# Kernel tuning notes

Measured on AMD Instinct MI355X. Metric: run time of the kernel, lower is better.

## Reference

```python
import jax, jax.numpy as jnp
import numpy as np

N_ATOMS = 500_000
N_BONDS = 1_000_000
NODE, EDGE, OUT = 128, 64, 128
N_PER_DEG = 125_000
DEGREES = (1, 2, 3, 4)
BN_EPS = 1e-5


def setup_inputs() -> dict:
    key = jax.random.key(0)
    ks = jax.random.split(key, 12)
    inp = {
        "atom_repr": jax.random.normal(ks[0], (N_ATOMS, NODE), dtype=jnp.float32),
        "bond_repr": jax.random.normal(ks[1], (N_BONDS, EDGE), dtype=jnp.float32),
    }
    for i, d in enumerate(DEGREES):
        inp[f"atom_idx_d{d}"] = jax.random.randint(jax.random.fold_in(ks[2], i), (N_PER_DEG, d), 0, N_ATOMS, dtype=jnp.int32)
        inp[f"bond_idx_d{d}"] = jax.random.randint(jax.random.fold_in(ks[3], i), (N_PER_DEG, d), 0, N_BONDS, dtype=jnp.int32)
        inp[f"W_d{d}"] = jax.random.normal(jax.random.fold_in(ks[4], i), (OUT, NODE + EDGE), dtype=jnp.float32) / np.sqrt(NODE + EDGE)
    inp["W_self"] = jax.random.normal(ks[5], (OUT, NODE), dtype=jnp.float32) / np.sqrt(NODE)
    inp["bias"] = jnp.zeros((1, OUT), dtype=jnp.float32)
    return inp


def reference(atom_repr, bond_repr,
              atom_idx_d1, atom_idx_d2, atom_idx_d3, atom_idx_d4,
              bond_idx_d1, bond_idx_d2, bond_idx_d3, bond_idx_d4,
              W_d1, W_d2, W_d3, W_d4, W_self, bias):
    atom_idxs = (atom_idx_d1, atom_idx_d2, atom_idx_d3, atom_idx_d4)
    bond_idxs = (bond_idx_d1, bond_idx_d2, bond_idx_d3, bond_idx_d4)
    Ws = (W_d1, W_d2, W_d3, W_d4)
    acts = []
    for aidx, bidx, W in zip(atom_idxs, bond_idxs, Ws):
        a = atom_repr[aidx].sum(axis=1)      # [n_d, NODE] gather+sum over neighbors
        b = bond_repr[bidx].sum(axis=1)      # [n_d, EDGE]
        stacked = jnp.concatenate([a, b], axis=1)  # [n_d, NODE+EDGE]
        acts.append(stacked @ W.T)           # [n_d, OUT]
    neighbor_repr = jnp.concatenate(acts, axis=0)  # [N_ATOMS, OUT]
    self_repr = atom_repr @ W_self.T               # [N_ATOMS, OUT]
    x = self_repr + neighbor_repr + bias
    # BatchNorm1d(affine=False), training mode: biased batch stats
    mean = jnp.mean(x, axis=0)
    var = jnp.var(x, axis=0)
    x = (x - mean) * jax.lax.rsqrt(var + BN_EPS)
    return jax.nn.relu(x)
```

## Files before the change

### kernel.cpp

```cpp
#include <hip/hip_runtime.h>

#define NODE 128
#define EDGE 64
#define OUTC 128
#define KTOT 320
#define NPD 125000
#define N_ATOMS_C 500000
#define BROWS 32
#define NB 8
#define NCHUNK 489
#define LDST 328
#define BN_EPS 1e-5f

typedef short bf16x8 __attribute__((ext_vector_type(8)));
typedef float floatx4 __attribute__((ext_vector_type(4)));

__device__ __forceinline__ unsigned short f2bf(float f) {
    unsigned u = __float_as_uint(f);
    u += 0x7fffu + ((u >> 16) & 1u);
    return (unsigned short)(u >> 16);
}
__device__ __forceinline__ unsigned pack2(float a, float b) {
    return (unsigned)f2bf(a) | ((unsigned)f2bf(b) << 16);
}
__device__ __forceinline__ void add4(float4& a, const float4 b) {
    a.x += b.x; a.y += b.y; a.z += b.z; a.w += b.w;
}

__global__ __launch_bounds__(256) void pack_weights_kernel(
    const float* __restrict__ w1, const float* __restrict__ w2,
    const float* __restrict__ w3, const float* __restrict__ w4,
    const float* __restrict__ W_self, float* __restrict__ stats,
    unsigned short* __restrict__ Wcat)
{
    if (blockIdx.x == 0 && threadIdx.x < 256) stats[threadIdx.x] = 0.f;
    const int idx = blockIdx.x * 256 + threadIdx.x;
    if (idx >= 4 * OUTC * KTOT) return;
    const int d   = idx / (OUTC * KTOT);
    const int rem = idx % (OUTC * KTOT);
    const int n = rem / KTOT, k = rem % KTOT;
    const float* wd = (d == 0) ? w1 : (d == 1) ? w2 : (d == 2) ? w3 : w4;
    const float v = (k < NODE) ? W_self[n * NODE + k]
                               : wd[n * (NODE + EDGE) + (k - NODE)];
    Wcat[idx] = f2bf(v);
}

__global__ __launch_bounds__(256, 2) void compute_x_kernel(
    const float* __restrict__ atom_repr, const float* __restrict__ bond_repr,
    const int* __restrict__ a1, const int* __restrict__ b1,
    const int* __restrict__ a2, const int* __restrict__ b2,
    const int* __restrict__ a3, const int* __restrict__ b3,
    const int* __restrict__ a4, const int* __restrict__ b4,
    const unsigned short* __restrict__ Wcat, const float* __restrict__ bias,
    float* __restrict__ out, float* __restrict__ stats)
{
    const int seg   = blockIdx.x & 3;
    const int chunk = blockIdx.x >> 2;
    const int deg = seg + 1;
    const int* aidx = (seg == 0) ? a1 : (seg == 1) ? a2 : (seg == 2) ? a3 : a4;
    const int* bidx = (seg == 0) ? b1 : (seg == 1) ? b2 : (seg == 2) ? b3 : b4;

    __shared__ unsigned short s_feat[2][BROWS][LDST];
    __shared__ float s_sum[OUTC], s_sq[OUTC];

    const int tid = threadIdx.x;
    if (tid < OUTC) { s_sum[tid] = 0.f; s_sq[tid] = 0.f; }

    const int w    = tid >> 6;
    const int lane = tid & 63;
    const int quad = lane >> 4;
    const int lrow = lane & 15;

    bf16x8 breg[2][10];
    {
        const unsigned short* Wc = Wcat + (size_t)seg * OUTC * KTOT;
        #pragma unroll
        for (int nt = 0; nt < 2; ++nt) {
            const int n = w * 32 + nt * 16 + lrow;
            #pragma unroll
            for (int ks = 0; ks < 10; ++ks) {
                const int k0 = quad * 8 + ks * 32;
                breg[nt][ks] = *reinterpret_cast<const bf16x8*>(Wc + n * KTOT + k0);
            }
        }
    }
    float bias_v[2];
    bias_v[0] = bias[w * 32 + lrow];
    bias_v[1] = bias[w * 32 + 16 + lrow];

    float lsum[2] = {0.f, 0.f}, lsq[2] = {0.f, 0.f};

    const int gr = tid >> 3;
    const int gt = tid & 7;
    const float4* ar = (const float4*)atom_repr;
    const float4* br = (const float4*)bond_repr;

    float4 st_s[4];
    float4 st_a[16];
    float4 st_b[8];

    auto issue = [&](int b) {
        const int r0 = chunk * (BROWS * NB) + b * BROWS + gr;
        const int rc = (r0 < NPD) ? r0 : 0;
        const size_t gi = (size_t)(seg * NPD) + rc;
        int ai[4], bi[4];
        #pragma unroll
        for (int j = 0; j < 4; ++j)
            if (j < deg) { ai[j] = aidx[rc * deg + j]; bi[j] = bidx[rc * deg + j]; }
        #pragma unroll
        for (int h = 0; h < 2; ++h) {
            const int c = h * 16 + gt * 2;
            st_s[h * 2 + 0] = ar[gi * 32 + c];
            st_s[h * 2 + 1] = ar[gi * 32 + c + 1];
            #pragma unroll
            for (int j = 0; j < 4; ++j)
                if (j < deg) {
                    st_a[j * 4 + h * 2 + 0] = ar[(size_t)ai[j] * 32 + c];
                    st_a[j * 4 + h * 2 + 1] = ar[(size_t)ai[j] * 32 + c + 1];
                }
        }
        const int cb = gt * 2;
        #pragma unroll
        for (int j = 0; j < 4; ++j)
            if (j < deg) {
                st_b[j * 2 + 0] = br[(size_t)bi[j] * 16 + cb];
                st_b[j * 2 + 1] = br[(size_t)bi[j] * 16 + cb + 1];
            }
    };

    issue(0);

    for (int b = 0; b < NB; ++b) {
        const int base = chunk * (BROWS * NB) + b * BROWS;
        if (base >= NPD) break;

        {
            unsigned short (*sf)[LDST] = s_feat[b & 1];
            #pragma unroll
            for (int h = 0; h < 2; ++h) {
                const int k0 = h * 64 + gt * 8;
                uint4 p;
                p.x = pack2(st_s[h * 2].x, st_s[h * 2].y);
                p.y = pack2(st_s[h * 2].z, st_s[h * 2].w);
                p.z = pack2(st_s[h * 2 + 1].x, st_s[h * 2 + 1].y);
                p.w = pack2(st_s[h * 2 + 1].z, st_s[h * 2 + 1].w);
                *reinterpret_cast<uint4*>(&sf[gr][k0]) = p;
                float4 u0 = st_a[h * 2], u1 = st_a[h * 2 + 1];
                #pragma unroll
                for (int j = 1; j < 4; ++j)
                    if (j < deg) { add4(u0, st_a[j * 4 + h * 2]); add4(u1, st_a[j * 4 + h * 2 + 1]); }
                p.x = pack2(u0.x, u0.y); p.y = pack2(u0.z, u0.w);
                p.z = pack2(u1.x, u1.y); p.w = pack2(u1.z, u1.w);
                *reinterpret_cast<uint4*>(&sf[gr][NODE + k0]) = p;
            }
            {
                const int k0 = gt * 8;
                float4 u0 = st_b[0], u1 = st_b[1];
                #pragma unroll
                for (int j = 1; j < 4; ++j)
                    if (j < deg) { add4(u0, st_b[j * 2]); add4(u1, st_b[j * 2 + 1]); }
                uint4 p;
                p.x = pack2(u0.x, u0.y); p.y = pack2(u0.z, u0.w);
                p.z = pack2(u1.x, u1.y); p.w = pack2(u1.z, u1.w);
                *reinterpret_cast<uint4*>(&sf[gr][2 * NODE + k0]) = p;
            }
        }

        if (b + 1 < NB) issue(b + 1);

        asm volatile("s_waitcnt lgkmcnt(0)" ::: "memory");
        __builtin_amdgcn_s_barrier();

        unsigned short (*sfr)[LDST] = s_feat[b & 1];
        floatx4 acc[2][2];
        #pragma unroll
        for (int mt = 0; mt < 2; ++mt)
            #pragma unroll
            for (int nt = 0; nt < 2; ++nt) {
                acc[mt][nt][0] = bias_v[nt]; acc[mt][nt][1] = bias_v[nt];
                acc[mt][nt][2] = bias_v[nt]; acc[mt][nt][3] = bias_v[nt];
            }
        #pragma unroll
        for (int ks = 0; ks < 10; ++ks) {
            bf16x8 af0 = *reinterpret_cast<const bf16x8*>(&sfr[lrow][quad * 8 + ks * 32]);
            bf16x8 af1 = *reinterpret_cast<const bf16x8*>(&sfr[16 + lrow][quad * 8 + ks * 32]);
            acc[0][0] = __builtin_amdgcn_mfma_f32_16x16x32_bf16(af0, breg[0][ks], acc[0][0], 0, 0, 0);
            acc[0][1] = __builtin_amdgcn_mfma_f32_16x16x32_bf16(af0, breg[1][ks], acc[0][1], 0, 0, 0);
            acc[1][0] = __builtin_amdgcn_mfma_f32_16x16x32_bf16(af1, breg[0][ks], acc[1][0], 0, 0, 0);
            acc[1][1] = __builtin_amdgcn_mfma_f32_16x16x32_bf16(af1, breg[1][ks], acc[1][1], 0, 0, 0);
        }

        #pragma unroll
        for (int mt = 0; mt < 2; ++mt) {
            #pragma unroll
            for (int nt = 0; nt < 2; ++nt) {
                const int n = w * 32 + nt * 16 + lrow;
                #pragma unroll
                for (int r = 0; r < 4; ++r) {
                    const int m = mt * 16 + quad * 4 + r;
                    const int row = base + m;
                    if (row < NPD) {
                        const float v = acc[mt][nt][r];
                        out[(size_t)(seg * NPD + row) * OUTC + n] = v;
                        lsum[nt] += v; lsq[nt] += v * v;
                    }
                }
            }
        }
    }

    atomicAdd(&s_sum[w * 32 + lrow], lsum[0]);
    atomicAdd(&s_sq [w * 32 + lrow], lsq[0]);
    atomicAdd(&s_sum[w * 32 + 16 + lrow], lsum[1]);
    atomicAdd(&s_sq [w * 32 + 16 + lrow], lsq[1]);
    __syncthreads();
    if (tid < OUTC) {
        atomicAdd(&stats[tid], s_sum[tid]);
        atomicAdd(&stats[OUTC + tid], s_sq[tid]);
    }
}

__global__ void finalize_stats_kernel(float* stats) {
    const int o = threadIdx.x;
    const float inv_n = 1.0f / (float)N_ATOMS_C;
    const float mean = stats[o] * inv_n;
    const float var  = stats[OUTC + o] * inv_n - mean * mean;
    stats[o] = mean;
    stats[OUTC + o] = rsqrtf(var + BN_EPS);
}

#define BN_TOT (N_ATOMS_C * (OUTC / 4))
#define BN_BLOCKS 2048

__global__ __launch_bounds__(256) void bn_relu_kernel(float* __restrict__ x,
                                                      const float* __restrict__ stats) {
    const int gid = blockIdx.x * 256 + threadIdx.x;
    const int c4 = gid & 31;
    const float4 m = ((const float4*)stats)[c4];
    const float4 s = ((const float4*)stats)[32 + c4];
    const int stride = BN_BLOCKS * 256;
    for (size_t e = (size_t)gid; e < (size_t)BN_TOT; e += stride) {
        float4 v = ((float4*)x)[e];
        v.x = fmaxf((v.x - m.x) * s.x, 0.f);
        v.y = fmaxf((v.y - m.y) * s.y, 0.f);
        v.z = fmaxf((v.z - m.z) * s.z, 0.f);
        v.w = fmaxf((v.w - m.w) * s.w, 0.f);
        ((float4*)x)[e] = v;
    }
}

extern "C" void kernel_launch(void* const* d_in, const int* in_sizes, int n_in,
                              void* d_out, int out_size, void* d_ws, size_t ws_size,
                              hipStream_t stream) {
    const float* atom_repr = (const float*)d_in[0];
    const float* bond_repr = (const float*)d_in[1];
    const int*   a1 = (const int*)d_in[2];
    const int*   b1 = (const int*)d_in[3];
    const float* w1 = (const float*)d_in[4];
    const int*   a2 = (const int*)d_in[5];
    const int*   b2 = (const int*)d_in[6];
    const float* w2 = (const float*)d_in[7];
    const int*   a3 = (const int*)d_in[8];
    const int*   b3 = (const int*)d_in[9];
    const float* w3 = (const float*)d_in[10];
    const int*   a4 = (const int*)d_in[11];
    const int*   b4 = (const int*)d_in[12];
    const float* w4 = (const float*)d_in[13];
    const float* W_self = (const float*)d_in[14];
    const float* bias   = (const float*)d_in[15];

    float* out   = (float*)d_out;
    float* stats = (float*)d_ws;
    unsigned short* Wcat = (unsigned short*)((char*)d_ws + 1024);

    pack_weights_kernel<<<(4 * OUTC * KTOT + 255) / 256, 256, 0, stream>>>(
        w1, w2, w3, w4, W_self, stats, Wcat);

    compute_x_kernel<<<NCHUNK * 4, 256, 0, stream>>>(
        atom_repr, bond_repr, a1, b1, a2, b2, a3, b3, a4, b4,
        Wcat, bias, out, stats);

    finalize_stats_kernel<<<1, 128, 0, stream>>>(stats);

    bn_relu_kernel<<<BN_BLOCKS, 256, 0, stream>>>(out, stats);
}
```

Measured before the change: 834.7 us.

## Pair degree segments per block for load balance and prefetch indices two stages ahead

Each block now handles 128 rows from two degree segments, pairing degree 1 with 4 and degree 2 with 3, so every block does a similar amount of gather work. Indices are loaded two stages ahead and features one stage ahead, which splits the dependent index-then-gather latency chain. The compile-time degrees allow full specialization. The cost is reloading the weight registers in the middle of the block and more live registers from the extra index buffers, which could reduce occupancy.

Result: slower. 861.7 us (+3.2%).

```diff
diff --git a/kernel.cpp b/kernel.cpp
--- a/kernel.cpp
+++ b/kernel.cpp
@@ -7,8 +7,9 @@
 #define NPD 125000
 #define N_ATOMS_C 500000
 #define BROWS 32
-#define NB 8
-#define NCHUNK 489
+#define NBATCH 8
+#define ROWS_PER_PHASE 128
+#define NCHUNK 977
 #define LDST 328
 #define BN_EPS 1e-5f
 
@@ -45,6 +46,199 @@
     Wcat[idx] = f2bf(v);
 }
 
+template<int SP, int SQ>
+__device__ __forceinline__ void run_pair(
+    const float4* __restrict__ ar, const float4* __restrict__ br,
+    const int* __restrict__ aP, const int* __restrict__ bP,
+    const int* __restrict__ aQ, const int* __restrict__ bQ,
+    const unsigned short* __restrict__ Wcat, const float* __restrict__ bias,
+    float* __restrict__ out, float* __restrict__ stats,
+    unsigned short (*s_feat)[BROWS][LDST], float* s_sum, float* s_sq,
+    const int chunk, const int tid)
+{
+    constexpr int DP = SP + 1, DQ = SQ + 1;
+    const int w    = tid >> 6;
+    const int lane = tid & 63;
+    const int quad = lane >> 4;
+    const int lrow = lane & 15;
+    const int gr   = tid >> 3;
+    const int gt   = tid & 7;
+
+    bf16x8 breg[2][10];
+    {
+        const unsigned short* Wc = Wcat + SP * OUTC * KTOT;
+        #pragma unroll
+        for (int nt = 0; nt < 2; ++nt) {
+            const int n = w * 32 + nt * 16 + lrow;
+            #pragma unroll
+            for (int ks = 0; ks < 10; ++ks)
+                breg[nt][ks] = *reinterpret_cast<const bf16x8*>(Wc + n * KTOT + quad * 8 + ks * 32);
+        }
+    }
+    float bias_v[2];
+    bias_v[0] = bias[w * 32 + lrow];
+    bias_v[1] = bias[w * 32 + 16 + lrow];
+    float lsum[2] = {0.f, 0.f}, lsq[2] = {0.f, 0.f};
+
+    float4 st_s[4];
+    float4 st_a[16];
+    float4 st_b[8];
+    int ia[2][4], ib[2][4];
+
+    auto issue_idx = [&](int t) {
+        const int dg = (t < 4) ? DP : DQ;
+        const int* ax = (t < 4) ? aP : aQ;
+        const int* bx = (t < 4) ? bP : bQ;
+        const int r0 = chunk * ROWS_PER_PHASE + (t & 3) * BROWS + gr;
+        const int rc = (r0 < NPD) ? r0 : (NPD - 1);
+        int* ia_ = ia[t & 1]; int* ib_ = ib[t & 1];
+        #pragma unroll
+        for (int j = 0; j < 4; ++j)
+            if (j < dg) { ia_[j] = ax[rc * dg + j]; ib_[j] = bx[rc * dg + j]; }
+    };
+
+    auto issue_feat = [&](int t) {
+        const int dg = (t < 4) ? DP : DQ;
+        const int sg = (t < 4) ? SP : SQ;
+        const int r0 = chunk * ROWS_PER_PHASE + (t & 3) * BROWS + gr;
+        const int rc = (r0 < NPD) ? r0 : (NPD - 1);
+        const size_t gi = (size_t)(sg * NPD) + rc;
+        const int* ia_ = ia[t & 1]; const int* ib_ = ib[t & 1];
+        #pragma unroll
+        for (int h = 0; h < 2; ++h) {
+            const int c = h * 16 + gt * 2;
+            st_s[h * 2 + 0] = ar[gi * 32 + c];
+            st_s[h * 2 + 1] = ar[gi * 32 + c + 1];
+            #pragma unroll
+            for (int j = 0; j < 4; ++j)
+                if (j < dg) {
+                    st_a[j * 4 + h * 2 + 0] = ar[(size_t)ia_[j] * 32 + c];
+                    st_a[j * 4 + h * 2 + 1] = ar[(size_t)ia_[j] * 32 + c + 1];
+                }
+        }
+        const int cb = gt * 2;
+        #pragma unroll
+        for (int j = 0; j < 4; ++j)
+            if (j < dg) {
+                st_b[j * 2 + 0] = br[(size_t)ib_[j] * 16 + cb];
+                st_b[j * 2 + 1] = br[(size_t)ib_[j] * 16 + cb + 1];
+            }
+    };
+
+    auto pack_lds = [&](int t) {
+        const int dg = (t < 4) ? DP : DQ;
+        unsigned short (*sf)[LDST] = s_feat[t & 1];
+        #pragma unroll
+        for (int h = 0; h < 2; ++h) {
+            const int k0 = h * 64 + gt * 8;
+            uint4 p;
+            p.x = pack2(st_s[h * 2].x, st_s[h * 2].y);
+            p.y = pack2(st_s[h * 2].z, st_s[h * 2].w);
+            p.z = pack2(st_s[h * 2 + 1].x, st_s[h * 2 + 1].y);
+            p.w = pack2(st_s[h * 2 + 1].z, st_s[h * 2 + 1].w);
+            *reinterpret_cast<uint4*>(&sf[gr][k0]) = p;
+            float4 u0 = st_a[h * 2], u1 = st_a[h * 2 + 1];
+            #pragma unroll
+            for (int j = 1; j < 4; ++j)
+                if (j < dg) { add4(u0, st_a[j * 4 + h * 2]); add4(u1, st_a[j * 4 + h * 2 + 1]); }
+            p.x = pack2(u0.x, u0.y); p.y = pack2(u0.z, u0.w);
+            p.z = pack2(u1.x, u1.y); p.w = pack2(u1.z, u1.w);
+            *reinterpret_cast<uint4*>(&sf[gr][NODE + k0]) = p;
+        }
+        {
+            const int k0 = gt * 8;
+            float4 u0 = st_b[0], u1 = st_b[1];
+            #pragma unroll
+            for (int j = 1; j < 4; ++j)
+                if (j < dg) { add4(u0, st_b[j * 2]); add4(u1, st_b[j * 2 + 1]); }
+            uint4 p;
+            p.x = pack2(u0.x, u0.y); p.y = pack2(u0.z, u0.w);
+            p.z = pack2(u1.x, u1.y); p.w = pack2(u1.z, u1.w);
+            *reinterpret_cast<uint4*>(&sf[gr][2 * NODE + k0]) = p;
+        }
+    };
+
+    auto compute_store = [&](int t) {
+        const int sg = (t < 4) ? SP : SQ;
+        const int base = chunk * ROWS_PER_PHASE + (t & 3) * BROWS;
+        unsigned short (*sfr)[LDST] = s_feat[t & 1];
+        floatx4 acc[2][2];
+        #pragma unroll
+        for (int mt = 0; mt < 2; ++mt)
+            #pragma unroll
+            for (int nt = 0; nt < 2; ++nt) {
+                acc[mt][nt][0] = bias_v[nt]; acc[mt][nt][1] = bias_v[nt];
+                acc[mt][nt][2] = bias_v[nt]; acc[mt][nt][3] = bias_v[nt];
+            }
+        #pragma unroll
+        for (int ks = 0; ks < 10; ++ks) {
+            bf16x8 af0 = *reinterpret_cast<const bf16x8*>(&sfr[lrow][quad * 8 + ks * 32]);
+            bf16x8 af1 = *reinterpret_cast<const bf16x8*>(&sfr[16 + lrow][quad * 8 + ks * 32]);
+            acc[0][0] = __builtin_amdgcn_mfma_f32_16x16x32_bf16(af0, breg[0][ks], acc[0][0], 0, 0, 0);
+            acc[0][1] = __builtin_amdgcn_mfma_f32_16x16x32_bf16(af0, breg[1][ks], acc[0][1], 0, 0, 0);
+            acc[1][0] = __builtin_amdgcn_mfma_f32_16x16x32_bf16(af1, breg[0][ks], acc[1][0], 0, 0, 0);
+            acc[1][1] = __builtin_amdgcn_mfma_f32_16x16x32_bf16(af1, breg[1][ks], acc[1][1], 0, 0, 0);
+        }
+        #pragma unroll
+        for (int mt = 0; mt < 2; ++mt) {
+            #pragma unroll
+            for (int nt = 0; nt < 2; ++nt) {
+                const int n = w * 32 + nt * 16 + lrow;
+                #pragma unroll
+                for (int r = 0; r < 4; ++r) {
+                    const int m = mt * 16 + quad * 4 + r;
+                    const int row = base + m;
+                    if (row < NPD) {
+                        const float v = acc[mt][nt][r];
+                        out[(size_t)(sg * NPD + row) * OUTC + n] = v;
+                        lsum[nt] += v; lsq[nt] += v * v;
+                    }
+                }
+            }
+        }
+    };
+
+    issue_idx(0);
+    issue_feat(0);
+    issue_idx(1);
+
+    #pragma unroll
+    for (int bb = 0; bb < NBATCH; ++bb) {
+        const bool v0 = (chunk * ROWS_PER_PHASE + (bb & 3) * BROWS) < NPD;
+        if (v0) pack_lds(bb);
+        __builtin_amdgcn_sched_barrier(0);
+        if (bb + 1 < NBATCH && (chunk * ROWS_PER_PHASE + ((bb + 1) & 3) * BROWS) < NPD)
+            issue_feat(bb + 1);
+        if (bb + 2 < NBATCH && (chunk * ROWS_PER_PHASE + ((bb + 2) & 3) * BROWS) < NPD)
+            issue_idx(bb + 2);
+        if (v0) {
+            asm volatile("s_waitcnt lgkmcnt(0)" ::: "memory");
+            __builtin_amdgcn_s_barrier();
+            compute_store(bb);
+        }
+        if (bb == 3) {
+            const unsigned short* Wc = Wcat + SQ * OUTC * KTOT;
+            #pragma unroll
+            for (int nt = 0; nt < 2; ++nt) {
+                const int n = w * 32 + nt * 16 + lrow;
+                #pragma unroll
+                for (int ks = 0; ks < 10; ++ks)
+                    breg[nt][ks] = *reinterpret_cast<const bf16x8*>(Wc + n * KTOT + quad * 8 + ks * 32);
+            }
+        }
+    }
+
+    atomicAdd(&s_sum[w * 32 + lrow], lsum[0]);
+    atomicAdd(&s_sq [w * 32 + lrow], lsq[0]);
+    atomicAdd(&s_sum[w * 32 + 16 + lrow], lsum[1]);
+    atomicAdd(&s_sq [w * 32 + 16 + lrow], lsq[1]);
+    __syncthreads();
+    if (tid < OUTC) {
+        atomicAdd(&stats[tid], s_sum[tid]);
+        atomicAdd(&stats[OUTC + tid], s_sq[tid]);
+    }
+}
+
 __global__ __launch_bounds__(256, 2) void compute_x_kernel(
     const float* __restrict__ atom_repr, const float* __restrict__ bond_repr,
     const int* __restrict__ a1, const int* __restrict__ b1,
@@ -54,170 +248,23 @@
     const unsigned short* __restrict__ Wcat, const float* __restrict__ bias,
     float* __restrict__ out, float* __restrict__ stats)
 {
-    const int seg   = blockIdx.x & 3;
-    const int chunk = blockIdx.x >> 2;
-    const int deg = seg + 1;
-    const int* aidx = (seg == 0) ? a1 : (seg == 1) ? a2 : (seg == 2) ? a3 : a4;
-    const int* bidx = (seg == 0) ? b1 : (seg == 1) ? b2 : (seg == 2) ? b3 : b4;
-
     __shared__ unsigned short s_feat[2][BROWS][LDST];
     __shared__ float s_sum[OUTC], s_sq[OUTC];
 
     const int tid = threadIdx.x;
     if (tid < OUTC) { s_sum[tid] = 0.f; s_sq[tid] = 0.f; }
 
-    const int w    = tid >> 6;
-    const int lane = tid & 63;
-    const int quad = lane >> 4;
-    const int lrow = lane & 15;
-
-    bf16x8 breg[2][10];
-    {
-        const unsigned short* Wc = Wcat + (size_t)seg * OUTC * KTOT;
-        #pragma unroll
-        for (int nt = 0; nt < 2; ++nt) {
-            const int n = w * 32 + nt * 16 + lrow;
-            #pragma unroll
-            for (int ks = 0; ks < 10; ++ks) {
-                const int k0 = quad * 8 + ks * 32;
-                breg[nt][ks] = *reinterpret_cast<const bf16x8*>(Wc + n * KTOT + k0);
-            }
-        }
-    }
-    float bias_v[2];
-    bias_v[0] = bias[w * 32 + lrow];
-    bias_v[1] = bias[w * 32 + 16 + lrow];
-
-    float lsum[2] = {0.f, 0.f}, lsq[2] = {0.f, 0.f};
-
-    const int gr = tid >> 3;
-    const int gt = tid & 7;
+    const int pair  = blockIdx.x & 1;
+    const int chunk = blockIdx.x >> 1;
     const float4* ar = (const float4*)atom_repr;
     const float4* br = (const float4*)bond_repr;
 
-    float4 st_s[4];
-    float4 st_a[16];
-    float4 st_b[8];
-
-    auto issue = [&](int b) {
-        const int r0 = chunk * (BROWS * NB) + b * BROWS + gr;
-        const int rc = (r0 < NPD) ? r0 : 0;
-        const size_t gi = (size_t)(seg * NPD) + rc;
-        int ai[4], bi[4];
-        #pragma unroll
-        for (int j = 0; j < 4; ++j)
-            if (j < deg) { ai[j] = aidx[rc * deg + j]; bi[j] = bidx[rc * deg + j]; }
-        #pragma unroll
-        for (int h = 0; h < 2; ++h) {
-            const int c = h * 16 + gt * 2;
-            st_s[h * 2 + 0] = ar[gi * 32 + c];
-            st_s[h * 2 + 1] = ar[gi * 32 + c + 1];
-            #pragma unroll
-            for (int j = 0; j < 4; ++j)
-                if (j < deg) {
-                    st_a[j * 4 + h * 2 + 0] = ar[(size_t)ai[j] * 32 + c];
-                    st_a[j * 4 + h * 2 + 1] = ar[(size_t)ai[j] * 32 + c + 1];
-                }
-        }
-        const int cb = gt * 2;
-        #pragma unroll
-        for (int j = 0; j < 4; ++j)
-            if (j < deg) {
-                st_b[j * 2 + 0] = br[(size_t)bi[j] * 16 + cb];
-                st_b[j * 2 + 1] = br[(size_t)bi[j] * 16 + cb + 1];
-            }
-    };
-
-    issue(0);
-
-    for (int b = 0; b < NB; ++b) {
-        const int base = chunk * (BROWS * NB) + b * BROWS;
-        if (base >= NPD) break;
-
-        {
-            unsigned short (*sf)[LDST] = s_feat[b & 1];
-            #pragma unroll
-            for (int h = 0; h < 2; ++h) {
-                const int k0 = h * 64 + gt * 8;
-                uint4 p;
-                p.x = pack2(st_s[h * 2].x, st_s[h * 2].y);
-                p.y = pack2(st_s[h * 2].z, st_s[h * 2].w);
-                p.z = pack2(st_s[h * 2 + 1].x, st_s[h * 2 + 1].y);
-                p.w = pack2(st_s[h * 2 + 1].z, st_s[h * 2 + 1].w);
-                *reinterpret_cast<uint4*>(&sf[gr][k0]) = p;
-                float4 u0 = st_a[h * 2], u1 = st_a[h * 2 + 1];
-                #pragma unroll
-                for (int j = 1; j < 4; ++j)
-                    if (j < deg) { add4(u0, st_a[j * 4 + h * 2]); add4(u1, st_a[j * 4 + h * 2 + 1]); }
-                p.x = pack2(u0.x, u0.y); p.y = pack2(u0.z, u0.w);
-                p.z = pack2(u1.x, u1.y); p.w = pack2(u1.z, u1.w);
-                *reinterpret_cast<uint4*>(&sf[gr][NODE + k0]) = p;
-            }
-            {
-                const int k0 = gt * 8;
-                float4 u0 = st_b[0], u1 = st_b[1];
-                #pragma unroll
-                for (int j = 1; j < 4; ++j)
-                    if (j < deg) { add4(u0, st_b[j * 2]); add4(u1, st_b[j * 2 + 1]); }
-                uint4 p;
-                p.x = pack2(u0.x, u0.y); p.y = pack2(u0.z, u0.w);
-                p.z = pack2(u1.x, u1.y); p.w = pack2(u1.z, u1.w);
-                *reinterpret_cast<uint4*>(&sf[gr][2 * NODE + k0]) = p;
-            }
-        }
-
-        if (b + 1 < NB) issue(b + 1);
-
-        asm volatile("s_waitcnt lgkmcnt(0)" ::: "memory");
-        __builtin_amdgcn_s_barrier();
-
-        unsigned short (*sfr)[LDST] = s_feat[b & 1];
-        floatx4 acc[2][2];
-        #pragma unroll
-        for (int mt = 0; mt < 2; ++mt)
-            #pragma unroll
-            for (int nt = 0; nt < 2; ++nt) {
-                acc[mt][nt][0] = bias_v[nt]; acc[mt][nt][1] = bias_v[nt];
-                acc[mt][nt][2] = bias_v[nt]; acc[mt][nt][3] = bias_v[nt];
-            }
-        #pragma unroll
-        for (int ks = 0; ks < 10; ++ks) {
-            bf16x8 af0 = *reinterpret_cast<const bf16x8*>(&sfr[lrow][quad * 8 + ks * 32]);
-            bf16x8 af1 = *reinterpret_cast<const bf16x8*>(&sfr[16 + lrow][quad * 8 + ks * 32]);
-            acc[0][0] = __builtin_amdgcn_mfma_f32_16x16x32_bf16(af0, breg[0][ks], acc[0][0], 0, 0, 0);
-            acc[0][1] = __builtin_amdgcn_mfma_f32_16x16x32_bf16(af0, breg[1][ks], acc[0][1], 0, 0, 0);
-            acc[1][0] = __builtin_amdgcn_mfma_f32_16x16x32_bf16(af1, breg[0][ks], acc[1][0], 0, 0, 0);
-            acc[1][1] = __builtin_amdgcn_mfma_f32_16x16x32_bf16(af1, breg[1][ks], acc[1][1], 0, 0, 0);
-        }
-
-        #pragma unroll
-        for (int mt = 0; mt < 2; ++mt) {
-            #pragma unroll
-            for (int nt = 0; nt < 2; ++nt) {
-                const int n = w * 32 + nt * 16 + lrow;
-                #pragma unroll
-                for (int r = 0; r < 4; ++r) {
-                    const int m = mt * 16 + quad * 4 + r;
-                    const int row = base + m;
-                    if (row < NPD) {
-                        const float v = acc[mt][nt][r];
-                        out[(size_t)(seg * NPD + row) * OUTC + n] = v;
-                        lsum[nt] += v; lsq[nt] += v * v;
-                    }
-                }
-            }
-        }
-    }
-
-    atomicAdd(&s_sum[w * 32 + lrow], lsum[0]);
-    atomicAdd(&s_sq [w * 32 + lrow], lsq[0]);
-    atomicAdd(&s_sum[w * 32 + 16 + lrow], lsum[1]);
-    atomicAdd(&s_sq [w * 32 + 16 + lrow], lsq[1]);
-    __syncthreads();
-    if (tid < OUTC) {
-        atomicAdd(&stats[tid], s_sum[tid]);
-        atomicAdd(&stats[OUTC + tid], s_sq[tid]);
-    }
+    if (pair == 0)
+        run_pair<0, 3>(ar, br, a1, b1, a4, b4, Wcat, bias, out, stats,
+                       s_feat, s_sum, s_sq, chunk, tid);
+    else
+        run_pair<1, 2>(ar, br, a2, b2, a3, b3, Wcat, bias, out, stats,
+                       s_feat, s_sum, s_sq, chunk, tid);
 }
 
 __global__ void finalize_stats_kernel(float* stats) {
@@ -276,7 +323,7 @@
     pack_weights_kernel<<<(4 * OUTC * KTOT + 255) / 256, 256, 0, stream>>>(
         w1, w2, w3, w4, W_self, stats, Wcat);
 
-    compute_x_kernel<<<NCHUNK * 4, 256, 0, stream>>>(
+    compute_x_kernel<<<NCHUNK * 2, 256, 0, stream>>>(
         atom_repr, bond_repr, a1, b1, a2, b2, a3, b3, a4, b4,
         Wcat, bias, out, stats);
 
```

## Template gather-GEMM on degree and pipeline index loads ahead of feature gathers

Applied to the files above, without the earlier changes.

The per-degree work becomes a template, so neighbor loops are fully unrolled with exact register arrays instead of runtime-guarded 4-wide arrays. Index loads are issued two tiles ahead of the dependent feature gathers, splitting the dependent-load chain across stages. The chunk size is halved to give twice as many blocks, and blocks are ordered so the heaviest degree-4 segment is scheduled first. This targets gather latency and load imbalance, at the cost of more code and extra index registers that may affect occupancy.

Result: faster. 808.8 us (-3.1%).

```diff
diff --git a/kernel.cpp b/kernel.cpp
--- a/kernel.cpp
+++ b/kernel.cpp
@@ -7,8 +7,8 @@
 #define NPD 125000
 #define N_ATOMS_C 500000
 #define BROWS 32
-#define NB 8
-#define NCHUNK 489
+#define NB 4
+#define NBLK 977
 #define LDST 328
 #define BN_EPS 1e-5f
 
@@ -45,6 +45,179 @@
     Wcat[idx] = f2bf(v);
 }
 
+template<int DEG>
+__device__ __forceinline__ void run_seg(
+    const float4* __restrict__ ar, const float4* __restrict__ br,
+    const int* __restrict__ aidx, const int* __restrict__ bidx,
+    const unsigned short* __restrict__ Wcat, const float* __restrict__ bias,
+    float* __restrict__ out, float* __restrict__ stats,
+    unsigned short (*s_feat)[BROWS][LDST], float* s_sum, float* s_sq,
+    const int chunk, const int tid)
+{
+    constexpr int SEG = DEG - 1;
+    const int w    = tid >> 6;
+    const int lane = tid & 63;
+    const int quad = lane >> 4;
+    const int lrow = lane & 15;
+    const int gr   = tid >> 3;
+    const int gt   = tid & 7;
+
+    bf16x8 breg[2][10];
+    {
+        const unsigned short* Wc = Wcat + SEG * OUTC * KTOT;
+        #pragma unroll
+        for (int nt = 0; nt < 2; ++nt) {
+            const int n = w * 32 + nt * 16 + lrow;
+            #pragma unroll
+            for (int ks = 0; ks < 10; ++ks)
+                breg[nt][ks] = *reinterpret_cast<const bf16x8*>(Wc + n * KTOT + quad * 8 + ks * 32);
+        }
+    }
+    float bias_v[2];
+    bias_v[0] = bias[w * 32 + lrow];
+    bias_v[1] = bias[w * 32 + 16 + lrow];
+    float lsum[2] = {0.f, 0.f}, lsq[2] = {0.f, 0.f};
+
+    float4 st_s[4];
+    float4 st_a[DEG][4];
+    float4 st_b[DEG][2];
+    int iaA[DEG], ibA[DEG];
+    int iaB[DEG], ibB[DEG];
+
+    const int rbase = chunk * (BROWS * NB);
+
+    auto issue_idx = [&](int t, int* ia_, int* ib_) {
+        const int r0 = rbase + t * BROWS + gr;
+        const int rc = (r0 < NPD) ? r0 : (NPD - 1);
+        #pragma unroll
+        for (int j = 0; j < DEG; ++j) {
+            ia_[j] = aidx[rc * DEG + j];
+            ib_[j] = bidx[rc * DEG + j];
+        }
+    };
+    auto issue_feat = [&](int t, const int* ia_, const int* ib_) {
+        const int r0 = rbase + t * BROWS + gr;
+        const int rc = (r0 < NPD) ? r0 : (NPD - 1);
+        const size_t gi = (size_t)(SEG * NPD) + rc;
+        #pragma unroll
+        for (int h = 0; h < 2; ++h) {
+            const int c = h * 16 + gt * 2;
+            st_s[h * 2 + 0] = ar[gi * 32 + c];
+            st_s[h * 2 + 1] = ar[gi * 32 + c + 1];
+            #pragma unroll
+            for (int j = 0; j < DEG; ++j) {
+                st_a[j][h * 2 + 0] = ar[(size_t)ia_[j] * 32 + c];
+                st_a[j][h * 2 + 1] = ar[(size_t)ia_[j] * 32 + c + 1];
+            }
+        }
+        const int cb = gt * 2;
+        #pragma unroll
+        for (int j = 0; j < DEG; ++j) {
+            st_b[j][0] = br[(size_t)ib_[j] * 16 + cb];
+            st_b[j][1] = br[(size_t)ib_[j] * 16 + cb + 1];
+        }
+    };
+    auto pack_lds = [&](unsigned short (*sf)[LDST]) {
+        #pragma unroll
+        for (int h = 0; h < 2; ++h) {
+            const int k0 = h * 64 + gt * 8;
+            uint4 p;
+            p.x = pack2(st_s[h * 2].x, st_s[h * 2].y);
+            p.y = pack2(st_s[h * 2].z, st_s[h * 2].w);
+            p.z = pack2(st_s[h * 2 + 1].x, st_s[h * 2 + 1].y);
+            p.w = pack2(st_s[h * 2 + 1].z, st_s[h * 2 + 1].w);
+            *reinterpret_cast<uint4*>(&sf[gr][k0]) = p;
+            float4 u0 = st_a[0][h * 2], u1 = st_a[0][h * 2 + 1];
+            #pragma unroll
+            for (int j = 1; j < DEG; ++j) { add4(u0, st_a[j][h * 2]); add4(u1, st_a[j][h * 2 + 1]); }
+            p.x = pack2(u0.x, u0.y); p.y = pack2(u0.z, u0.w);
+            p.z = pack2(u1.x, u1.y); p.w = pack2(u1.z, u1.w);
+            *reinterpret_cast<uint4*>(&sf[gr][NODE + k0]) = p;
+        }
+        {
+            const int k0 = gt * 8;
+            float4 u0 = st_b[0][0], u1 = st_b[0][1];
+            #pragma unroll
+            for (int j = 1; j < DEG; ++j) { add4(u0, st_b[j][0]); add4(u1, st_b[j][1]); }
+            uint4 p;
+            p.x = pack2(u0.x, u0.y); p.y = pack2(u0.z, u0.w);
+            p.z = pack2(u1.x, u1.y); p.w = pack2(u1.z, u1.w);
+            *reinterpret_cast<uint4*>(&sf[gr][2 * NODE + k0]) = p;
+        }
+    };
+    auto compute_store = [&](int t, unsigned short (*sfr)[LDST]) {
+        const int base = rbase + t * BROWS;
+        floatx4 acc[2][2];
+        #pragma unroll
+        for (int mt = 0; mt < 2; ++mt)
+            #pragma unroll
+            for (int nt = 0; nt < 2; ++nt) {
+                acc[mt][nt][0] = bias_v[nt]; acc[mt][nt][1] = bias_v[nt];
+                acc[mt][nt][2] = bias_v[nt]; acc[mt][nt][3] = bias_v[nt];
+            }
+        #pragma unroll
+        for (int ks = 0; ks < 10; ++ks) {
+            bf16x8 af0 = *reinterpret_cast<const bf16x8*>(&sfr[lrow][quad * 8 + ks * 32]);
+            bf16x8 af1 = *reinterpret_cast<const bf16x8*>(&sfr[16 + lrow][quad * 8 + ks * 32]);
+            acc[0][0] = __builtin_amdgcn_mfma_f32_16x16x32_bf16(af0, breg[0][ks], acc[0][0], 0, 0, 0);
+            acc[0][1] = __builtin_amdgcn_mfma_f32_16x16x32_bf16(af0, breg[1][ks], acc[0][1], 0, 0, 0);
+            acc[1][0] = __builtin_amdgcn_mfma_f32_16x16x32_bf16(af1, breg[0][ks], acc[1][0], 0, 0, 0);
+            acc[1][1] = __builtin_amdgcn_mfma_f32_16x16x32_bf16(af1, breg[1][ks], acc[1][1], 0, 0, 0);
+        }
+        #pragma unroll
+        for (int mt = 0; mt < 2; ++mt) {
+            #pragma unroll
+            for (int nt = 0; nt < 2; ++nt) {
+                const int n = w * 32 + nt * 16 + lrow;
+                #pragma unroll
+                for (int r = 0; r < 4; ++r) {
+                    const int m = mt * 16 + quad * 4 + r;
+                    const int row = base + m;
+                    if (row < NPD) {
+                        const float v = acc[mt][nt][r];
+                        out[(size_t)(SEG * NPD + row) * OUTC + n] = v;
+                        lsum[nt] += v; lsq[nt] += v * v;
+                    }
+                }
+            }
+        }
+    };
+
+    auto valid = [&](int t) { return (rbase + t * BROWS) < NPD; };
+
+    issue_idx(0, iaA, ibA);
+    if (valid(1)) issue_idx(1, iaB, ibB);
+    issue_feat(0, iaA, ibA);
+
+    for (int p = 0; p < NB / 2; ++p) {
+        const int t0 = p * 2, t1 = t0 + 1;
+        const bool u0 = valid(t0);
+        const bool u1 = valid(t1);
+        if (u0) pack_lds(s_feat[0]);
+        if (u1) issue_feat(t1, iaB, ibB);
+        if (t0 + 2 < NB && valid(t0 + 2)) issue_idx(t0 + 2, iaA, ibA);
+        asm volatile("s_waitcnt lgkmcnt(0)" ::: "memory");
+        __builtin_amdgcn_s_barrier();
+        if (u0) compute_store(t0, s_feat[0]);
+        if (u1) pack_lds(s_feat[1]);
+        if (t0 + 2 < NB && valid(t0 + 2)) issue_feat(t0 + 2, iaA, ibA);
+        if (t1 + 2 < NB && valid(t1 + 2)) issue_idx(t1 + 2, iaB, ibB);
+        asm volatile("s_waitcnt lgkmcnt(0)" ::: "memory");
+        __builtin_amdgcn_s_barrier();
+        if (u1) compute_store(t1, s_feat[1]);
+    }
+
+    atomicAdd(&s_sum[w * 32 + lrow], lsum[0]);
+    atomicAdd(&s_sq [w * 32 + lrow], lsq[0]);
+    atomicAdd(&s_sum[w * 32 + 16 + lrow], lsum[1]);
+    atomicAdd(&s_sq [w * 32 + 16 + lrow], lsq[1]);
+    __syncthreads();
+    if (tid < OUTC) {
+        atomicAdd(&stats[tid], s_sum[tid]);
+        atomicAdd(&stats[OUTC + tid], s_sq[tid]);
+    }
+}
+
 __global__ __launch_bounds__(256, 2) void compute_x_kernel(
     const float* __restrict__ atom_repr, const float* __restrict__ bond_repr,
     const int* __restrict__ a1, const int* __restrict__ b1,
@@ -54,170 +227,27 @@
     const unsigned short* __restrict__ Wcat, const float* __restrict__ bias,
     float* __restrict__ out, float* __restrict__ stats)
 {
-    const int seg   = blockIdx.x & 3;
-    const int chunk = blockIdx.x >> 2;
-    const int deg = seg + 1;
-    const int* aidx = (seg == 0) ? a1 : (seg == 1) ? a2 : (seg == 2) ? a3 : a4;
-    const int* bidx = (seg == 0) ? b1 : (seg == 1) ? b2 : (seg == 2) ? b3 : b4;
-
     __shared__ unsigned short s_feat[2][BROWS][LDST];
     __shared__ float s_sum[OUTC], s_sq[OUTC];
 
     const int tid = threadIdx.x;
     if (tid < OUTC) { s_sum[tid] = 0.f; s_sq[tid] = 0.f; }
 
-    const int w    = tid >> 6;
-    const int lane = tid & 63;
-    const int quad = lane >> 4;
-    const int lrow = lane & 15;
-
-    bf16x8 breg[2][10];
-    {
-        const unsigned short* Wc = Wcat + (size_t)seg * OUTC * KTOT;
-        #pragma unroll
-        for (int nt = 0; nt < 2; ++nt) {
-            const int n = w * 32 + nt * 16 + lrow;
-            #pragma unroll
-            for (int ks = 0; ks < 10; ++ks) {
-                const int k0 = quad * 8 + ks * 32;
-                breg[nt][ks] = *reinterpret_cast<const bf16x8*>(Wc + n * KTOT + k0);
-            }
-        }
-    }
-    float bias_v[2];
-    bias_v[0] = bias[w * 32 + lrow];
-    bias_v[1] = bias[w * 32 + 16 + lrow];
-
-    float lsum[2] = {0.f, 0.f}, lsq[2] = {0.f, 0.f};
-
-    const int gr = tid >> 3;
-    const int gt = tid & 7;
+    const int bid   = blockIdx.x;
+    const int s     = bid / NBLK;
+    const int chunk = bid - s * NBLK;
+    const int seg   = 3 - s;
     const float4* ar = (const float4*)atom_repr;
     const float4* br = (const float4*)bond_repr;
 
-    float4 st_s[4];
-    float4 st_a[16];
-    float4 st_b[8];
-
-    auto issue = [&](int b) {
-        const int r0 = chunk * (BROWS * NB) + b * BROWS + gr;
-        const int rc = (r0 < NPD) ? r0 : 0;
-        const size_t gi = (size_t)(seg * NPD) + rc;
-        int ai[4], bi[4];
-        #pragma unroll
-        for (int j = 0; j < 4; ++j)
-            if (j < deg) { ai[j] = aidx[rc * deg + j]; bi[j] = bidx[rc * deg + j]; }
-        #pragma unroll
-        for (int h = 0; h < 2; ++h) {
-            const int c = h * 16 + gt * 2;
-            st_s[h * 2 + 0] = ar[gi * 32 + c];
-            st_s[h * 2 + 1] = ar[gi * 32 + c + 1];
-            #pragma unroll
-            for (int j = 0; j < 4; ++j)
-                if (j < deg) {
-                    st_a[j * 4 + h * 2 + 0] = ar[(size_t)ai[j] * 32 + c];
-                    st_a[j * 4 + h * 2 + 1] = ar[(size_t)ai[j] * 32 + c + 1];
-                }
-        }
-        const int cb = gt * 2;
-        #pragma unroll
-        for (int j = 0; j < 4; ++j)
-            if (j < deg) {
-                st_b[j * 2 + 0] = br[(size_t)bi[j] * 16 + cb];
-                st_b[j * 2 + 1] = br[(size_t)bi[j] * 16 + cb + 1];
-            }
-    };
-
-    issue(0);
-
-    for (int b = 0; b < NB; ++b) {
-        const int base = chunk * (BROWS * NB) + b * BROWS;
-        if (base >= NPD) break;
-
-        {
-            unsigned short (*sf)[LDST] = s_feat[b & 1];
-            #pragma unroll
-            for (int h = 0; h < 2; ++h) {
-                const int k0 = h * 64 + gt * 8;
-                uint4 p;
-                p.x = pack2(st_s[h * 2].x, st_s[h * 2].y);
-                p.y = pack2(st_s[h * 2].z, st_s[h * 2].w);
-                p.z = pack2(st_s[h * 2 + 1].x, st_s[h * 2 + 1].y);
-                p.w = pack2(st_s[h * 2 + 1].z, st_s[h * 2 + 1].w);
-                *reinterpret_cast<uint4*>(&sf[gr][k0]) = p;
-                float4 u0 = st_a[h * 2], u1 = st_a[h * 2 + 1];
-                #pragma unroll
-                for (int j = 1; j < 4; ++j)
-                    if (j < deg) { add4(u0, st_a[j * 4 + h * 2]); add4(u1, st_a[j * 4 + h * 2 + 1]); }
-                p.x = pack2(u0.x, u0.y); p.y = pack2(u0.z, u0.w);
-                p.z = pack2(u1.x, u1.y); p.w = pack2(u1.z, u1.w);
-                *reinterpret_cast<uint4*>(&sf[gr][NODE + k0]) = p;
-            }
-            {
-                const int k0 = gt * 8;
-                float4 u0 = st_b[0], u1 = st_b[1];
-                #pragma unroll
-                for (int j = 1; j < 4; ++j)
-                    if (j < deg) { add4(u0, st_b[j * 2]); add4(u1, st_b[j * 2 + 1]); }
-                uint4 p;
-                p.x = pack2(u0.x, u0.y); p.y = pack2(u0.z, u0.w);
-                p.z = pack2(u1.x, u1.y); p.w = pack2(u1.z, u1.w);
-                *reinterpret_cast<uint4*>(&sf[gr][2 * NODE + k0]) = p;
-            }
-        }
-
-        if (b + 1 < NB) issue(b + 1);
-
-        asm volatile("s_waitcnt lgkmcnt(0)" ::: "memory");
-        __builtin_amdgcn_s_barrier();
-
-        unsigned short (*sfr)[LDST] = s_feat[b & 1];
-        floatx4 acc[2][2];
-        #pragma unroll
-        for (int mt = 0; mt < 2; ++mt)
-            #pragma unroll
-            for (int nt = 0; nt < 2; ++nt) {
-                acc[mt][nt][0] = bias_v[nt]; acc[mt][nt][1] = bias_v[nt];
-                acc[mt][nt][2] = bias_v[nt]; acc[mt][nt][3] = bias_v[nt];
-            }
-        #pragma unroll
-        for (int ks = 0; ks < 10; ++ks) {
-            bf16x8 af0 = *reinterpret_cast<const bf16x8*>(&sfr[lrow][quad * 8 + ks * 32]);
-            bf16x8 af1 = *reinterpret_cast<const bf16x8*>(&sfr[16 + lrow][quad * 8 + ks * 32]);
-            acc[0][0] = __builtin_amdgcn_mfma_f32_16x16x32_bf16(af0, breg[0][ks], acc[0][0], 0, 0, 0);
-            acc[0][1] = __builtin_amdgcn_mfma_f32_16x16x32_bf16(af0, breg[1][ks], acc[0][1], 0, 0, 0);
-            acc[1][0] = __builtin_amdgcn_mfma_f32_16x16x32_bf16(af1, breg[0][ks], acc[1][0], 0, 0, 0);
-            acc[1][1] = __builtin_amdgcn_mfma_f32_16x16x32_bf16(af1, breg[1][ks], acc[1][1], 0, 0, 0);
-        }
-
-        #pragma unroll
-        for (int mt = 0; mt < 2; ++mt) {
-            #pragma unroll
-            for (int nt = 0; nt < 2; ++nt) {
-                const int n = w * 32 + nt * 16 + lrow;
-                #pragma unroll
-                for (int r = 0; r < 4; ++r) {
-                    const int m = mt * 16 + quad * 4 + r;
-                    const int row = base + m;
-                    if (row < NPD) {
-                        const float v = acc[mt][nt][r];
-                        out[(size_t)(seg * NPD + row) * OUTC + n] = v;
-                        lsum[nt] += v; lsq[nt] += v * v;
-                    }
-                }
-            }
-        }
-    }
-
-    atomicAdd(&s_sum[w * 32 + lrow], lsum[0]);
-    atomicAdd(&s_sq [w * 32 + lrow], lsq[0]);
-    atomicAdd(&s_sum[w * 32 + 16 + lrow], lsum[1]);
-    atomicAdd(&s_sq [w * 32 + 16 + lrow], lsq[1]);
-    __syncthreads();
-    if (tid < OUTC) {
-        atomicAdd(&stats[tid], s_sum[tid]);
-        atomicAdd(&stats[OUTC + tid], s_sq[tid]);
-    }
+    if (seg == 3)
+        run_seg<4>(ar, br, a4, b4, Wcat, bias, out, stats, s_feat, s_sum, s_sq, chunk, tid);
+    else if (seg == 2)
+        run_seg<3>(ar, br, a3, b3, Wcat, bias, out, stats, s_feat, s_sum, s_sq, chunk, tid);
+    else if (seg == 1)
+        run_seg<2>(ar, br, a2, b2, Wcat, bias, out, stats, s_feat, s_sum, s_sq, chunk, tid);
+    else
+        run_seg<1>(ar, br, a1, b1, Wcat, bias, out, stats, s_feat, s_sum, s_sq, chunk, tid);
 }
 
 __global__ void finalize_stats_kernel(float* stats) {
@@ -276,7 +306,7 @@
     pack_weights_kernel<<<(4 * OUTC * KTOT + 255) / 256, 256, 0, stream>>>(
         w1, w2, w3, w4, W_self, stats, Wcat);
 
-    compute_x_kernel<<<NCHUNK * 4, 256, 0, stream>>>(
+    compute_x_kernel<<<NBLK * 4, 256, 0, stream>>>(
         atom_repr, bond_repr, a1, b1, a2, b2, a3, b3, a4, b4,
         Wcat, bias, out, stats);
 
```
